# Kernel tuning notes

Hardware: AMD Instinct MI355X
Metric: run time of the kernel (lower is better)

Reference implementation:

```python
import jax, jax.numpy as jnp
import numpy as np

B, T, C, H = 4, 2048, 1024, 16
HD = C // H  # head dim = 64


def setup_inputs() -> dict:
    key = jax.random.key(0)
    k1, k2, k3 = jax.random.split(key, 3)
    scale_in = 1.0 / np.sqrt(C)
    return {
        "x": jax.random.normal(k1, (B, T, C), dtype=jnp.float32),
        "W_attn": jax.random.normal(k2, (C, 3 * C), dtype=jnp.float32) * scale_in,
        "b_attn": jnp.zeros((3 * C,), dtype=jnp.float32),
        "W_proj": jax.random.normal(k3, (C, C), dtype=jnp.float32) * scale_in,
        "b_proj": jnp.zeros((C,), dtype=jnp.float32),
    }


def reference(x, W_attn, b_attn, W_proj, b_proj):
    b, t, c = x.shape
    qkv = x @ W_attn + b_attn                      # [B,T,3C]
    q, k, v = jnp.split(qkv, 3, axis=-1)
    # [B,T,C] -> [B,H,T,HD]
    def heads(z):
        return z.reshape(b, t, H, HD).transpose(0, 2, 1, 3)
    q, k, v = heads(q), heads(k), heads(v)
    att = jnp.einsum("bhqd,bhkd->bhqk", q, k) / jnp.sqrt(jnp.float32(HD))
    causal = jnp.tril(jnp.ones((t, t), dtype=bool))
    att = jnp.where(causal, att, -jnp.inf)
    att = jax.nn.softmax(att, axis=-1)             # dropout p=0 -> identity
    y = jnp.einsum("bhqk,bhkd->bhqd", att, v)      # [B,H,T,HD]
    y = y.transpose(0, 2, 1, 3).reshape(b, t, c)   # [B,T,C]
    return y @ W_proj + b_proj
```

## Files before the change

kernel.cpp:

```cpp
#include <hip/hip_runtime.h>
#include <hip/hip_bf16.h>

typedef unsigned int u32;
typedef unsigned short u16;
typedef __bf16 bf16x8 __attribute__((ext_vector_type(8)));
typedef float f32x4 __attribute__((ext_vector_type(4)));
typedef _Float16 f16;
typedef _Float16 f16x2 __attribute__((ext_vector_type(2)));
typedef _Float16 f16x4 __attribute__((ext_vector_type(4)));

#define B_ 4
#define T_ 2048
#define C_ 1024
#define H_ 16
#define HD_ 64
#define M_ (B_*T_)
#define N3C (3*C_)

__device__ __forceinline__ u16 f2bf(float f) {
  u32 u = __builtin_bit_cast(u32, f);
  u = (u + 0x7fffu + ((u >> 16) & 1u)) >> 16;
  return (u16)u;
}

#define GLD16(gp, lp) __builtin_amdgcn_global_load_lds( \
    (const __attribute__((address_space(1))) u32*)(gp), \
    (__attribute__((address_space(3))) u32*)(lp), 16, 0, 0)

#if __has_builtin(__builtin_amdgcn_exp2f)
#define EXP2F(x) __builtin_amdgcn_exp2f(x)
#else
#define EXP2F(x) exp2f(x)
#endif

__global__ __launch_bounds__(256) void prep(
    const float* __restrict__ x, const float* __restrict__ Wa,
    const float* __restrict__ Wp,
    u16* __restrict__ xb, u16* __restrict__ W1t, u16* __restrict__ W2t) {
  __shared__ float t[32][33];
  const int blk = blockIdx.x, tid = threadIdx.x;
  if (blk < 8192) {
    int i = blk * 256 + tid;
    float4 v = ((const float4*)x)[i];
    ushort4 o;
    o.x = f2bf(v.x); o.y = f2bf(v.y); o.z = f2bf(v.z); o.w = f2bf(v.w);
    ((ushort4*)xb)[i] = o;
    return;
  }
  const float* W; u16* Wt; int Ndim, id;
  if (blk < 8192 + 3072) { W = Wa; Wt = W1t; Ndim = N3C; id = blk - 8192; }
  else                   { W = Wp; Wt = W2t; Ndim = C_;  id = blk - 11264; }
  const int nt = Ndim / 32;
  const int n0 = (id % nt) * 32, k0 = (id / nt) * 32;
  const int tx = tid & 31, ty = tid >> 5;
  #pragma unroll
  for (int i = ty; i < 32; i += 8)
    t[i][tx] = W[(long)(k0 + i) * Ndim + n0 + tx];
  __syncthreads();
  #pragma unroll
  for (int i = ty; i < 32; i += 8)
    Wt[(long)(n0 + i) * C_ + k0 + tx] = f2bf(t[tx][i]);
}

__global__ __launch_bounds__(256) void transpose_v(
    const u16* __restrict__ qkv, f16* __restrict__ vt) {
  const int t0 = blockIdx.x * 64, bh = blockIdx.y;
  const int b = bh >> 4, h = bh & 15;
  const int t = threadIdx.x & 63, dq = threadIdx.x >> 6;
  #pragma unroll
  for (int p = 0; p < 4; ++p) {
    int d0 = (p * 4 + dq) * 4;
    ushort4 v = *(const ushort4*)&qkv[
        ((long)(b * T_ + t0 + t)) * N3C + 2 * C_ + h * 64 + d0];
    const u16* vp = (const u16*)&v;
    #pragma unroll
    for (int j = 0; j < 4; ++j) {
      float f = __builtin_bit_cast(float, ((u32)vp[j]) << 16);
      vt[((long)bh * 64 + d0 + j) * T_ + t0 + t] = (f16)f;
    }
  }
}

template<int WRITE_BF16>
__global__ __launch_bounds__(256) void gemm_bt(
    const u16* __restrict__ A, const u16* __restrict__ Bt,
    const float* __restrict__ bias, void* __restrict__ Cout,
    int N, int K) {
  __shared__ u16 As[128 * 64];
  __shared__ u16 Bs[128 * 64];
  const int tid = threadIdx.x;
  const int wave = tid >> 6, lane = tid & 63;
  const int wm = wave >> 1, wn = wave & 1;
  const int l15 = lane & 15, quad = lane >> 4;
  const int rA = lane >> 3, cxor = (lane & 7) ^ rA;
  const long rowA0 = (long)blockIdx.x * 128;
  const long colB0 = (long)blockIdx.y * 128;

  f32x4 acc[4][4] = {};

  const u16* Ag = A + (rowA0 + wave * 32 + rA) * K + cxor * 8;
  const u16* Bg = Bt + (colB0 + wave * 32 + rA) * K + cxor * 8;
  u16* Asw = &As[(wave * 32) * 64];
  u16* Bsw = &Bs[(wave * 32) * 64];

  for (int k0 = 0; k0 < K; k0 += 64) {
    #pragma unroll
    for (int j = 0; j < 4; ++j) {
      GLD16(Ag + (long)j * 8 * K + k0, Asw + j * 8 * 64);
      GLD16(Bg + (long)j * 8 * K + k0, Bsw + j * 8 * 64);
    }
    __syncthreads();
    #pragma unroll
    for (int kk = 0; kk < 2; ++kk) {
      bf16x8 af[4], bfr[4];
      #pragma unroll
      for (int mt = 0; mt < 4; ++mt) {
        int r = wm * 64 + mt * 16 + l15;
        int c = (kk * 4 + quad) ^ (r & 7);
        af[mt] = *(const bf16x8*)&As[r * 64 + c * 8];
      }
      #pragma unroll
      for (int nt = 0; nt < 4; ++nt) {
        int r = wn * 64 + nt * 16 + l15;
        int c = (kk * 4 + quad) ^ (r & 7);
        bfr[nt] = *(const bf16x8*)&Bs[r * 64 + c * 8];
      }
      #pragma unroll
      for (int mt = 0; mt < 4; ++mt)
        #pragma unroll
        for (int nt = 0; nt < 4; ++nt)
          acc[mt][nt] = __builtin_amdgcn_mfma_f32_16x16x32_bf16(
              af[mt], bfr[nt], acc[mt][nt], 0, 0, 0);
    }
    __syncthreads();
  }

  float bl[4];
  #pragma unroll
  for (int nt = 0; nt < 4; ++nt)
    bl[nt] = bias[colB0 + wn * 64 + nt * 16 + l15];
  #pragma unroll
  for (int mt = 0; mt < 4; ++mt) {
    long row = rowA0 + wm * 64 + mt * 16 + quad * 4;
    #pragma unroll
    for (int nt = 0; nt < 4; ++nt) {
      long col = colB0 + wn * 64 + nt * 16 + l15;
      #pragma unroll
      for (int r = 0; r < 4; ++r) {
        float v = acc[mt][nt][r] + bl[nt];
        if (WRITE_BF16) ((u16*)Cout)[(row + r) * N + col] = f2bf(v);
        else            ((float*)Cout)[(row + r) * N + col] = v;
      }
    }
  }
}

__global__ __launch_bounds__(256, 6) void flash_attn(
    const u16* __restrict__ qkv, const f16* __restrict__ vt,
    u16* __restrict__ yb) {
  __shared__ u16 Ks[2][64 * 64];
  __shared__ f16 Vts[64 * 72];
  const int bx = blockIdx.x;
  const int bh = blockIdx.y;
  const int b = bh >> 4, h = bh & 15;
  const int tid = threadIdx.x, wave = tid >> 6, lane = tid & 63;
  const int l15 = lane & 15, quad = lane >> 4;
  const int rA = lane >> 3, cxor = (lane & 7) ^ rA;

  const u16* Qb = qkv + (long)b * T_ * N3C + h * HD_;
  const f16* Vb = vt + (long)bh * HD_ * T_;
  const u16* Kb0 = Qb + C_ + (long)(wave * 16 + rA) * N3C + cxor * 8;

  const int rv = tid >> 3;
  const int c16 = tid & 7;

  const float cs = 0.125f * 1.44269504088896340736f;

  #pragma unroll 1
  for (int pass = 0; pass < 2; ++pass) {
    const int qt = pass ? bx : 31 - bx;
    const int nKT = qt + 1;
    const int qrow = qt * 64 + wave * 16 + l15;
    const bf16x8 bq0 = *(const bf16x8*)&Qb[(long)qrow * N3C + quad * 8];
    const bf16x8 bq1 = *(const bf16x8*)&Qb[(long)qrow * N3C + 32 + quad * 8];

    float qq = 0.f;
    #pragma unroll
    for (int j = 0; j < 8; ++j) {
      float a = (float)bq0[j], bv = (float)bq1[j];
      qq = __builtin_fmaf(a, a, qq);
      qq = __builtin_fmaf(bv, bv, qq);
    }
    qq += __shfl_xor(qq, 16);
    qq += __shfl_xor(qq, 32);
    const float nref = -qq * cs;

    const u16* kp = Kb0;
    const f16* vp = Vb + (long)rv * T_ + c16 * 8;

    __syncthreads();
    GLD16(kp, &Ks[0][(wave * 16) * 64]);
    GLD16(kp + 8 * N3C, &Ks[0][(wave * 16 + 8) * 64]);
    kp += 64 * N3C;
    uint4 vn0 = *(const uint4*)vp;
    uint4 vn1 = *(const uint4*)(vp + 32 * T_);
    vp += 64;

    float li = 0.f;
    f32x4 o[4] = {};

    for (int kt = 0; kt < nKT; ++kt) {
      const int buf = kt & 1;
      __syncthreads();
      *(uint4*)&Vts[rv * 72 + c16 * 8] = vn0;
      *(uint4*)&Vts[(rv + 32) * 72 + c16 * 8] = vn1;
      __syncthreads();

      if (kt + 1 < nKT) {
        GLD16(kp, &Ks[buf ^ 1][(wave * 16) * 64]);
        GLD16(kp + 8 * N3C, &Ks[buf ^ 1][(wave * 16 + 8) * 64]);
        kp += 64 * N3C;
        vn0 = *(const uint4*)vp;
        vn1 = *(const uint4*)(vp + 32 * T_);
        vp += 64;
      }

      f32x4 St[4] = {};
      #pragma unroll
      for (int kk = 0; kk < 2; ++kk) {
        bf16x8 qf = kk ? bq1 : bq0;
        #pragma unroll
        for (int mt = 0; mt < 4; ++mt) {
          int r = mt * 16 + l15;
          int c = (kk * 4 + quad) ^ (l15 & 7);
          bf16x8 kf = *(const bf16x8*)&Ks[buf][r * 64 + c * 8];
          St[mt] = __builtin_amdgcn_mfma_f32_16x16x32_bf16(kf, qf, St[mt], 0, 0, 0);
        }
      }

      if (kt == qt) {
        #pragma unroll
        for (int mt = 0; mt < 4; ++mt)
          #pragma unroll
          for (int r = 0; r < 4; ++r)
            if (mt * 16 + quad * 4 + r > wave * 16 + l15)
              St[mt][r] = -__builtin_inff();
      }

      float ps = 0.f;
      f16x4 pf[4];
      #pragma unroll
      for (int mt = 0; mt < 4; ++mt) {
        float p0 = EXP2F(__builtin_fmaf(St[mt][0], cs, nref));
        float p1 = EXP2F(__builtin_fmaf(St[mt][1], cs, nref));
        float p2 = EXP2F(__builtin_fmaf(St[mt][2], cs, nref));
        float p3 = EXP2F(__builtin_fmaf(St[mt][3], cs, nref));
        ps += (p0 + p1) + (p2 + p3);
        f16x2 lo = __builtin_bit_cast(f16x2, __builtin_amdgcn_cvt_pkrtz(p0, p1));
        f16x2 hi = __builtin_bit_cast(f16x2, __builtin_amdgcn_cvt_pkrtz(p2, p3));
        pf[mt][0] = lo[0]; pf[mt][1] = lo[1]; pf[mt][2] = hi[0]; pf[mt][3] = hi[1];
      }
      li += ps;

      #pragma unroll
      for (int dt = 0; dt < 4; ++dt) {
        #pragma unroll
        for (int kc = 0; kc < 4; ++kc) {
          f16x4 vf = *(const f16x4*)&Vts[(dt * 16 + l15) * 72 + kc * 16 + quad * 4];
          o[dt] = __builtin_amdgcn_mfma_f32_16x16x16f16(vf, pf[kc], o[dt], 0, 0, 0);
        }
      }
    }

    li += __shfl_xor(li, 16);
    li += __shfl_xor(li, 32);
    float inv = 1.f / li;
    #pragma unroll
    for (int dt = 0; dt < 4; ++dt) {
      ushort4 w;
      w.x = f2bf(o[dt][0] * inv);
      w.y = f2bf(o[dt][1] * inv);
      w.z = f2bf(o[dt][2] * inv);
      w.w = f2bf(o[dt][3] * inv);
      *(ushort4*)&yb[((long)b * T_ + qrow) * C_ + h * HD_ + dt * 16 + quad * 4] = w;
    }
  }
}

extern "C" void kernel_launch(void* const* d_in, const int* in_sizes, int n_in,
                              void* d_out, int out_size, void* d_ws, size_t ws_size,
                              hipStream_t stream) {
  const float* x      = (const float*)d_in[0];
  const float* W_attn = (const float*)d_in[1];
  const float* b_attn = (const float*)d_in[2];
  const float* W_proj = (const float*)d_in[3];
  const float* b_proj = (const float*)d_in[4];
  float* out = (float*)d_out;

  char* ws = (char*)d_ws;
  u16* xb   = (u16*)(ws);
  f16* vtb  = (f16*)(ws);
  u16* W1t  = (u16*)(ws + 16777216);
  u16* W2t  = (u16*)(ws + 23068672);
  u16* qkvb = (u16*)(ws + 25165824);
  u16* yb   = (u16*)(ws + 75497472);

  prep<<<dim3(12288), dim3(256), 0, stream>>>(x, W_attn, W_proj, xb, W1t, W2t);
  gemm_bt<1><<<dim3(M_ / 128, N3C / 128), dim3(256), 0, stream>>>(
      xb, W1t, b_attn, qkvb, N3C, C_);
  transpose_v<<<dim3(T_ / 64, B_ * H_), dim3(256), 0, stream>>>(qkvb, vtb);
  flash_attn<<<dim3(16, B_ * H_), dim3(256), 0, stream>>>(qkvb, vtb, yb);
  gemm_bt<0><<<dim3(M_ / 128, C_ / 128), dim3(256), 0, stream>>>(
      yb, W2t, b_proj, out, C_, C_);
}
```

Measured before the change: 280.0 us.

## Fuse V transpose into QKV GEMM epilogue and remap attention block order

The QKV GEMM epilogue now writes Q and K as bf16 into a narrower 2C-wide buffer and writes V directly as transposed f16 per head, which removes the separate transpose_v kernel and its extra read and write of V. Flash attention reads the narrower QK layout and uses a 1D grid with a remapped block index that groups heads and query tiles differently, presumably for better cache locality. The V epilogue stores are strided by T, so they may be less coalesced than before, and they use round-toward-zero f16 conversion.

```diff
diff --git a/kernel.cpp b/kernel.cpp
--- a/kernel.cpp
+++ b/kernel.cpp
@@ -16,6 +16,7 @@
 #define HD_ 64
 #define M_ (B_*T_)
 #define N3C (3*C_)
+#define N2C (2*C_)
 
 __device__ __forceinline__ u16 f2bf(float f) {
   u32 u = __builtin_bit_cast(u32, f);
@@ -62,30 +63,11 @@
     Wt[(long)(n0 + i) * C_ + k0 + tx] = f2bf(t[tx][i]);
 }
 
-__global__ __launch_bounds__(256) void transpose_v(
-    const u16* __restrict__ qkv, f16* __restrict__ vt) {
-  const int t0 = blockIdx.x * 64, bh = blockIdx.y;
-  const int b = bh >> 4, h = bh & 15;
-  const int t = threadIdx.x & 63, dq = threadIdx.x >> 6;
-  #pragma unroll
-  for (int p = 0; p < 4; ++p) {
-    int d0 = (p * 4 + dq) * 4;
-    ushort4 v = *(const ushort4*)&qkv[
-        ((long)(b * T_ + t0 + t)) * N3C + 2 * C_ + h * 64 + d0];
-    const u16* vp = (const u16*)&v;
-    #pragma unroll
-    for (int j = 0; j < 4; ++j) {
-      float f = __builtin_bit_cast(float, ((u32)vp[j]) << 16);
-      vt[((long)bh * 64 + d0 + j) * T_ + t0 + t] = (f16)f;
-    }
-  }
-}
-
-template<int WRITE_BF16>
+template<int MODE>
 __global__ __launch_bounds__(256) void gemm_bt(
     const u16* __restrict__ A, const u16* __restrict__ Bt,
     const float* __restrict__ bias, void* __restrict__ Cout,
-    int N, int K) {
+    f16* __restrict__ vt, int N, int K) {
   __shared__ u16 As[128 * 64];
   __shared__ u16 Bs[128 * 64];
   const int tid = threadIdx.x;
@@ -139,37 +121,60 @@
   #pragma unroll
   for (int nt = 0; nt < 4; ++nt)
     bl[nt] = bias[colB0 + wn * 64 + nt * 16 + l15];
+
+  const bool vmode = (MODE == 1) && (colB0 >= N2C);
   #pragma unroll
   for (int mt = 0; mt < 4; ++mt) {
     long row = rowA0 + wm * 64 + mt * 16 + quad * 4;
     #pragma unroll
     for (int nt = 0; nt < 4; ++nt) {
       long col = colB0 + wn * 64 + nt * 16 + l15;
-      #pragma unroll
-      for (int r = 0; r < 4; ++r) {
-        float v = acc[mt][nt][r] + bl[nt];
-        if (WRITE_BF16) ((u16*)Cout)[(row + r) * N + col] = f2bf(v);
-        else            ((float*)Cout)[(row + r) * N + col] = v;
+      float v0 = acc[mt][nt][0] + bl[nt];
+      float v1 = acc[mt][nt][1] + bl[nt];
+      float v2 = acc[mt][nt][2] + bl[nt];
+      float v3 = acc[mt][nt][3] + bl[nt];
+      if (MODE == 0) {
+        float* Cf = (float*)Cout;
+        Cf[(row + 0) * N + col] = v0;
+        Cf[(row + 1) * N + col] = v1;
+        Cf[(row + 2) * N + col] = v2;
+        Cf[(row + 3) * N + col] = v3;
+      } else if (!vmode) {
+        u16* qk = (u16*)Cout;
+        qk[(row + 0) * N2C + col] = f2bf(v0);
+        qk[(row + 1) * N2C + col] = f2bf(v1);
+        qk[(row + 2) * N2C + col] = f2bf(v2);
+        qk[(row + 3) * N2C + col] = f2bf(v3);
+      } else {
+        int cv = (int)(col - N2C);
+        int hh = cv >> 6, dd = cv & 63;
+        int bb = (int)(row >> 11);
+        long t = row & 2047;
+        f16x2 lo = __builtin_bit_cast(f16x2, __builtin_amdgcn_cvt_pkrtz(v0, v1));
+        f16x2 hi = __builtin_bit_cast(f16x2, __builtin_amdgcn_cvt_pkrtz(v2, v3));
+        f16x4 w; w[0] = lo[0]; w[1] = lo[1]; w[2] = hi[0]; w[3] = hi[1];
+        *(f16x4*)&vt[(((long)bb * H_ + hh) * HD_ + dd) * T_ + t] = w;
       }
     }
   }
 }
 
 __global__ __launch_bounds__(256, 6) void flash_attn(
-    const u16* __restrict__ qkv, const f16* __restrict__ vt,
+    const u16* __restrict__ qk, const f16* __restrict__ vt,
     u16* __restrict__ yb) {
   __shared__ u16 Ks[2][64 * 64];
   __shared__ f16 Vts[64 * 72];
-  const int bx = blockIdx.x;
-  const int bh = blockIdx.y;
+  const int l = blockIdx.x;
+  const int bh = (l & 7) | ((l >> 7) << 3);
+  const int bx = (l >> 3) & 15;
   const int b = bh >> 4, h = bh & 15;
   const int tid = threadIdx.x, wave = tid >> 6, lane = tid & 63;
   const int l15 = lane & 15, quad = lane >> 4;
   const int rA = lane >> 3, cxor = (lane & 7) ^ rA;
 
-  const u16* Qb = qkv + (long)b * T_ * N3C + h * HD_;
+  const u16* Qb = qk + (long)b * T_ * N2C + h * HD_;
   const f16* Vb = vt + (long)bh * HD_ * T_;
-  const u16* Kb0 = Qb + C_ + (long)(wave * 16 + rA) * N3C + cxor * 8;
+  const u16* Kb0 = Qb + C_ + (long)(wave * 16 + rA) * N2C + cxor * 8;
 
   const int rv = tid >> 3;
   const int c16 = tid & 7;
@@ -181,8 +186,8 @@
     const int qt = pass ? bx : 31 - bx;
     const int nKT = qt + 1;
     const int qrow = qt * 64 + wave * 16 + l15;
-    const bf16x8 bq0 = *(const bf16x8*)&Qb[(long)qrow * N3C + quad * 8];
-    const bf16x8 bq1 = *(const bf16x8*)&Qb[(long)qrow * N3C + 32 + quad * 8];
+    const bf16x8 bq0 = *(const bf16x8*)&Qb[(long)qrow * N2C + quad * 8];
+    const bf16x8 bq1 = *(const bf16x8*)&Qb[(long)qrow * N2C + 32 + quad * 8];
 
     float qq = 0.f;
     #pragma unroll
@@ -200,8 +205,8 @@
 
     __syncthreads();
     GLD16(kp, &Ks[0][(wave * 16) * 64]);
-    GLD16(kp + 8 * N3C, &Ks[0][(wave * 16 + 8) * 64]);
-    kp += 64 * N3C;
+    GLD16(kp + 8 * N2C, &Ks[0][(wave * 16 + 8) * 64]);
+    kp += 64 * N2C;
     uint4 vn0 = *(const uint4*)vp;
     uint4 vn1 = *(const uint4*)(vp + 32 * T_);
     vp += 64;
@@ -218,8 +223,8 @@
 
       if (kt + 1 < nKT) {
         GLD16(kp, &Ks[buf ^ 1][(wave * 16) * 64]);
-        GLD16(kp + 8 * N3C, &Ks[buf ^ 1][(wave * 16 + 8) * 64]);
-        kp += 64 * N3C;
+        GLD16(kp + 8 * N2C, &Ks[buf ^ 1][(wave * 16 + 8) * 64]);
+        kp += 64 * N2C;
         vn0 = *(const uint4*)vp;
         vn1 = *(const uint4*)(vp + 32 * T_);
         vp += 64;
@@ -299,17 +304,16 @@
 
   char* ws = (char*)d_ws;
   u16* xb   = (u16*)(ws);
-  f16* vtb  = (f16*)(ws);
   u16* W1t  = (u16*)(ws + 16777216);
   u16* W2t  = (u16*)(ws + 23068672);
-  u16* qkvb = (u16*)(ws + 25165824);
+  u16* qkb  = (u16*)(ws + 25165824);
+  f16* vtb  = (f16*)(ws + 58720256);
   u16* yb   = (u16*)(ws + 75497472);
 
   prep<<<dim3(12288), dim3(256), 0, stream>>>(x, W_attn, W_proj, xb, W1t, W2t);
   gemm_bt<1><<<dim3(M_ / 128, N3C / 128), dim3(256), 0, stream>>>(
-      xb, W1t, b_attn, qkvb, N3C, C_);
-  transpose_v<<<dim3(T_ / 64, B_ * H_), dim3(256), 0, stream>>>(qkvb, vtb);
-  flash_attn<<<dim3(16, B_ * H_), dim3(256), 0, stream>>>(qkvb, vtb, yb);
+      xb, W1t, b_attn, qkb, vtb, N3C, C_);
+  flash_attn<<<dim3(1024), dim3(256), 0, stream>>>(qkb, vtb, yb);
   gemm_bt<0><<<dim3(M_ / 128, C_ / 128), dim3(256), 0, stream>>>(
-      yb, W2t, b_proj, out, C_, C_);
-}
+      yb, W2t, b_proj, out, nullptr, C_, C_);
+}
```

Measured after the change: 254.8 us. -9.0%, faster.
